# Optimization experiments

Hardware: AMD Instinct MI355X
Metric: run time of the kernel (lower is better)

## Reference

```python
import jax, jax.numpy as jnp
import numpy as np

B, LD, HD, CC, SC, PN, MAX_N = 256, 256, 512, 64, 256, 100000, 128


def setup_inputs() -> dict:
    key = jax.random.key(0)
    ks = jax.random.split(key, 24)
    def W(k, i, o):
        return jax.random.normal(k, (i, o), jnp.float32) * 0.02
    latent = jax.random.normal(ks[0], (B, LD), jnp.float32)
    n = jax.random.randint(ks[1], (B,), 0, MAX_N, jnp.int32)
    points = jax.random.normal(ks[2], (PN, SC), jnp.float32)
    a = jax.random.normal(ks[3], (PN, CC), jnp.float32)
    angles_params = a / (jnp.linalg.norm(a, axis=1, keepdims=True) + 1e-5)
    return {
        "latent": latent, "n": n, "points": points, "angles_params": angles_params,
        # angle_mlp: LD->HD->HD->HD->CC (4 linears, relu between)
        "aw1": W(ks[4], LD, HD), "ab1": jnp.zeros((HD,), jnp.float32),
        "aw2": W(ks[5], HD, HD), "ab2": jnp.zeros((HD,), jnp.float32),
        "aw3": W(ks[6], HD, HD), "ab3": jnp.zeros((HD,), jnp.float32),
        "aw4": W(ks[7], HD, CC), "ab4": jnp.zeros((CC,), jnp.float32),
        # lin1/lin2: 1 -> SC
        "l1w": W(ks[8], 1, SC), "l1b": jnp.zeros((SC,), jnp.float32),
        "l2w": W(ks[9], 1, SC), "l2b": jnp.zeros((SC,), jnp.float32),
        # out_lin: (SC+LD)->(SC+LD)->SC->SC
        "ow1": W(ks[10], SC + LD, SC + LD), "ob1": jnp.zeros((SC + LD,), jnp.float32),
        "ow2": W(ks[11], SC + LD, SC), "ob2": jnp.zeros((SC,), jnp.float32),
        "ow3": W(ks[12], SC, SC), "ob3": jnp.zeros((SC,), jnp.float32),
    }


def reference(latent, n, points, angles_params,
              aw1, ab1, aw2, ab2, aw3, ab3, aw4, ab4,
              l1w, l1b, l2w, l2b,
              ow1, ob1, ow2, ob2, ow3, ob3):
    n_r = jnp.clip(n, 1, MAX_N)  # round_n
    # angle_mlp
    h = jax.nn.relu(latent @ aw1 + ab1)
    h = jax.nn.relu(h @ aw2 + ab2)
    h = jax.nn.relu(h @ aw3 + ab3)
    ang = h @ aw4 + ab4                                   # [B, CC]
    ang = ang / (jnp.linalg.norm(ang, axis=1, keepdims=True) + 1e-5)
    cosine = jax.nn.softmax(ang @ angles_params.T, axis=1)  # [B, PN]
    srted, idx = jax.lax.top_k(cosine, MAX_N)             # sorted descending
    sel = points[idx]                                     # [B, MAX_N, SC] gather
    s = (MAX_N * srted)[..., None]                        # [B, MAX_N, 1]
    alpha = s @ l1w + l1b
    beta = s @ l2w + l2b
    mod = alpha * sel + beta                              # [B, MAX_N, SC]
    mask = (jnp.arange(MAX_N)[None, :] < n_r[:, None]).astype(jnp.float32)[..., None]
    cat = jnp.concatenate(
        [mod, jnp.broadcast_to(latent[:, None, :], (latent.shape[0], MAX_N, latent.shape[1]))],
        axis=-1)
    o = jax.nn.relu(cat @ ow1 + ob1)
    o = jax.nn.relu(o @ ow2 + ob2)
    out = o @ ow3 + ob3                                   # [B, MAX_N, SC]
    return out, mask, n_r
```

## Files before the change

### kernel.cpp

```cpp
#include <hip/hip_runtime.h>

#define PN 100000
#define NCB2 1563
#define NCBG 782
#define TSEL 0.33f
#define NSLOT 8
#define PREP_AP 3128
#define PREP_TOT 4408
#define PREP_CHUNK 1102

typedef _Float16 f16;
typedef _Float16 f16x8 __attribute__((ext_vector_type(8)));
typedef _Float16 f16x4 __attribute__((ext_vector_type(4)));
typedef float f32x4 __attribute__((ext_vector_type(4)));

__device__ __forceinline__ unsigned int sortkey(float f) {
    unsigned int u = __float_as_uint(f);
    return u ^ ((u & 0x80000000u) ? 0xFFFFFFFFu : 0x80000000u);
}

__device__ __forceinline__ void gload_lds16(const void* g, void* l) {
    __builtin_amdgcn_global_load_lds((const __attribute__((address_space(1))) void*)g,
                                     (__attribute__((address_space(3))) void*)l, 16, 0, 0);
}

__device__ __forceinline__ void prep_work(
    int pid, const float* __restrict__ ap, f16* __restrict__ apHpre, f16* __restrict__ apLpre,
    const float* __restrict__ ow1, const float* __restrict__ ow2, const float* __restrict__ ow3,
    f16* __restrict__ W1t, f16* __restrict__ W2t, f16* __restrict__ W3t)
{
    if (pid < PREP_AP) {
        int idx = pid * 256 + threadIdx.x;
        int gcol = idx >> 3, m = idx & 7;
        int bx = gcol >> 7, col = gcol & 127;
        size_t woff = (size_t)bx * 16384 + (size_t)col * 128 + (size_t)((m ^ (col & 7)) << 4);
        f16x8 h, l;
        if (gcol < PN) {
            const float* src = &ap[(size_t)gcol * 64 + m * 8];
            float4 a = *(const float4*)&src[0];
            float4 b = *(const float4*)&src[4];
            h[0] = (f16)a.x; l[0] = (f16)(a.x - (float)h[0]);
            h[1] = (f16)a.y; l[1] = (f16)(a.y - (float)h[1]);
            h[2] = (f16)a.z; l[2] = (f16)(a.z - (float)h[2]);
            h[3] = (f16)a.w; l[3] = (f16)(a.w - (float)h[3]);
            h[4] = (f16)b.x; l[4] = (f16)(b.x - (float)h[4]);
            h[5] = (f16)b.y; l[5] = (f16)(b.y - (float)h[5]);
            h[6] = (f16)b.z; l[6] = (f16)(b.z - (float)h[6]);
            h[7] = (f16)b.w; l[7] = (f16)(b.w - (float)h[7]);
        } else {
            h = (f16x8){}; l = (f16x8){};
        }
        *(f16x8*)((char*)apHpre + woff) = h;
        *(f16x8*)((char*)apLpre + woff) = l;
    } else {
        int idx = (pid - PREP_AP) * 256 + threadIdx.x;
        if (idx < 131072) {
            int n = idx >> 8, k = idx & 255;
            W1t[idx] = (f16)ow1[(size_t)k * 512 + n];
        } else if (idx < 262144) {
            int j = idx - 131072;
            int n = j >> 9, k = j & 511;
            W2t[j] = (f16)ow2[(size_t)k * 256 + n];
        } else {
            int j = idx - 262144;
            int n = j >> 8, k = j & 255;
            W3t[j] = (f16)ow3[(size_t)k * 256 + n];
        }
    }
}

template<int RELU>
__global__ __launch_bounds__(256) void k1_layer(
    const float* __restrict__ X, const float* __restrict__ W,
    const float* __restrict__ bias, float* __restrict__ Y,
    int N, int K, int prep_base,
    const float* __restrict__ ap, f16* __restrict__ apHpre, f16* __restrict__ apLpre,
    const float* __restrict__ ow1, const float* __restrict__ ow2, const float* __restrict__ ow3,
    f16* __restrict__ W1t, f16* __restrict__ W2t, f16* __restrict__ W3t)
{
    int bid = blockIdx.x;
    if (bid >= 64) {
        prep_work(prep_base + bid - 64, ap, apHpre, apLpre, ow1, ow2, ow3, W1t, W2t, W3t);
        return;
    }
    __shared__ __align__(16) float As[128][36];
    __shared__ __align__(16) float Bs[128][68];
    int t = threadIdx.x;
    int cbase = (bid & 7) * 64;
    int rbase = (bid >> 3) * 32;
    int tx = t & 15, ty = t >> 4;
    float acc[2][4] = {};

    for (int kt = 0; kt < K; kt += 128) {
        #pragma unroll
        for (int i = 0; i < 4; ++i) {
            int e = i * 256 + t;
            int r = e >> 5, k4 = e & 31;
            float4 v = *(const float4*)&X[(size_t)(rbase + r) * K + kt + k4 * 4];
            As[k4 * 4 + 0][r] = v.x; As[k4 * 4 + 1][r] = v.y;
            As[k4 * 4 + 2][r] = v.z; As[k4 * 4 + 3][r] = v.w;
        }
        #pragma unroll
        for (int i = 0; i < 8; ++i) {
            int e = i * 256 + t;
            int k = e >> 4, c4 = e & 15;
            *(float4*)&Bs[k][c4 * 4] = *(const float4*)&W[(size_t)(kt + k) * N + cbase + c4 * 4];
        }
        __syncthreads();
        #pragma unroll 8
        for (int k = 0; k < 128; ++k) {
            float2 av = *(const float2*)&As[k][ty * 2];
            float4 bv = *(const float4*)&Bs[k][tx * 4];
            acc[0][0] = fmaf(av.x, bv.x, acc[0][0]); acc[0][1] = fmaf(av.x, bv.y, acc[0][1]);
            acc[0][2] = fmaf(av.x, bv.z, acc[0][2]); acc[0][3] = fmaf(av.x, bv.w, acc[0][3]);
            acc[1][0] = fmaf(av.y, bv.x, acc[1][0]); acc[1][1] = fmaf(av.y, bv.y, acc[1][1]);
            acc[1][2] = fmaf(av.y, bv.z, acc[1][2]); acc[1][3] = fmaf(av.y, bv.w, acc[1][3]);
        }
        __syncthreads();
    }
    #pragma unroll
    for (int i = 0; i < 2; ++i) {
        int row = rbase + ty * 2 + i;
        #pragma unroll
        for (int j = 0; j < 4; ++j) {
            int col = cbase + tx * 4 + j;
            float v = acc[i][j] + bias[col];
            Y[(size_t)row * N + col] = RELU ? fmaxf(v, 0.f) : v;
        }
    }
}

__global__ __launch_bounds__(256) void k1_tail(
    const float* __restrict__ X, const float* __restrict__ W4,
    const float* __restrict__ b4, f16* __restrict__ angH, f16* __restrict__ angL,
    const float* __restrict__ latent, const float* __restrict__ ow1lat,
    const float* __restrict__ ob1, float* __restrict__ Lc, int prep_base,
    const float* __restrict__ ap, f16* __restrict__ apHpre, f16* __restrict__ apLpre,
    const float* __restrict__ ow1, const float* __restrict__ ow2, const float* __restrict__ ow3,
    f16* __restrict__ W1t, f16* __restrict__ W2t, f16* __restrict__ W3t)
{
    if (blockIdx.x >= 72) {
        prep_work(prep_base + blockIdx.x - 72, ap, apHpre, apLpre, ow1, ow2, ow3, W1t, W2t, W3t);
        return;
    }
    __shared__ __align__(16) float As[128][36];
    __shared__ __align__(16) float Bs[128][68];
    int t = threadIdx.x;
    int tx = t & 15, ty = t >> 4;
    float acc[2][4] = {};

    if (blockIdx.x < 8) {
        int rbase = blockIdx.x * 32;
        for (int kt = 0; kt < 512; kt += 128) {
            #pragma unroll
            for (int i = 0; i < 4; ++i) {
                int e = i * 256 + t;
                int r = e >> 5, k4 = e & 31;
                float4 v = *(const float4*)&X[(size_t)(rbase + r) * 512 + kt + k4 * 4];
                As[k4 * 4 + 0][r] = v.x; As[k4 * 4 + 1][r] = v.y;
                As[k4 * 4 + 2][r] = v.z; As[k4 * 4 + 3][r] = v.w;
            }
            #pragma unroll
            for (int i = 0; i < 8; ++i) {
                int e = i * 256 + t;
                int k = e >> 4, c4 = e & 15;
                *(float4*)&Bs[k][c4 * 4] = *(const float4*)&W4[(size_t)(kt + k) * 64 + c4 * 4];
            }
            __syncthreads();
            #pragma unroll 8
            for (int k = 0; k < 128; ++k) {
                float2 av = *(const float2*)&As[k][ty * 2];
                float4 bv = *(const float4*)&Bs[k][tx * 4];
                acc[0][0] = fmaf(av.x, bv.x, acc[0][0]); acc[0][1] = fmaf(av.x, bv.y, acc[0][1]);
                acc[0][2] = fmaf(av.x, bv.z, acc[0][2]); acc[0][3] = fmaf(av.x, bv.w, acc[0][3]);
                acc[1][0] = fmaf(av.y, bv.x, acc[1][0]); acc[1][1] = fmaf(av.y, bv.y, acc[1][1]);
                acc[1][2] = fmaf(av.y, bv.z, acc[1][2]); acc[1][3] = fmaf(av.y, bv.w, acc[1][3]);
            }
            __syncthreads();
        }
        #pragma unroll
        for (int i = 0; i < 2; ++i) {
            float v[4];
            float ss = 0.f;
            #pragma unroll
            for (int j = 0; j < 4; ++j) {
                v[j] = acc[i][j] + b4[tx * 4 + j];
                ss = fmaf(v[j], v[j], ss);
            }
            ss += __shfl_xor(ss, 1); ss += __shfl_xor(ss, 2);
            ss += __shfl_xor(ss, 4); ss += __shfl_xor(ss, 8);
            float inv = 1.0f / (sqrtf(ss) + 1e-5f);
            int row = rbase + ty * 2 + i;
            f16x4 h, l;
            #pragma unroll
            for (int j = 0; j < 4; ++j) {
                float val = v[j] * inv;
                h[j] = (f16)val;
                l[j] = (f16)(val - (float)h[j]);
            }
            *(f16x4*)&angH[(size_t)row * 64 + tx * 4] = h;
            *(f16x4*)&angL[(size_t)row * 64 + tx * 4] = l;
        }
    } else {
        int bid = blockIdx.x - 8;
        int cbase = (bid & 7) * 64;
        int rbase = (bid >> 3) * 32;
        for (int kt = 0; kt < 256; kt += 128) {
            #pragma unroll
            for (int i = 0; i < 4; ++i) {
                int e = i * 256 + t;
                int r = e >> 5, k4 = e & 31;
                float4 v = *(const float4*)&latent[(size_t)(rbase + r) * 256 + kt + k4 * 4];
                As[k4 * 4 + 0][r] = v.x; As[k4 * 4 + 1][r] = v.y;
                As[k4 * 4 + 2][r] = v.z; As[k4 * 4 + 3][r] = v.w;
            }
            #pragma unroll
            for (int i = 0; i < 8; ++i) {
                int e = i * 256 + t;
                int k = e >> 4, c4 = e & 15;
                *(float4*)&Bs[k][c4 * 4] = *(const float4*)&ow1lat[(size_t)(kt + k) * 512 + cbase + c4 * 4];
            }
            __syncthreads();
            #pragma unroll 8
            for (int k = 0; k < 128; ++k) {
                float2 av = *(const float2*)&As[k][ty * 2];
                float4 bv = *(const float4*)&Bs[k][tx * 4];
                acc[0][0] = fmaf(av.x, bv.x, acc[0][0]); acc[0][1] = fmaf(av.x, bv.y, acc[0][1]);
                acc[0][2] = fmaf(av.x, bv.z, acc[0][2]); acc[0][3] = fmaf(av.x, bv.w, acc[0][3]);
                acc[1][0] = fmaf(av.y, bv.x, acc[1][0]); acc[1][1] = fmaf(av.y, bv.y, acc[1][1]);
                acc[1][2] = fmaf(av.y, bv.z, acc[1][2]); acc[1][3] = fmaf(av.y, bv.w, acc[1][3]);
            }
            __syncthreads();
        }
        #pragma unroll
        for (int i = 0; i < 2; ++i) {
            int row = rbase + ty * 2 + i;
            #pragma unroll
            for (int j = 0; j < 4; ++j) {
                int col = cbase + tx * 4 + j;
                Lc[(size_t)row * 512 + col] = acc[i][j] + ob1[col];
            }
        }
    }
}

__global__ __launch_bounds__(256) void k2v10(
    const f16* __restrict__ angH, const f16* __restrict__ angL,
    const f16* __restrict__ apHpre, const f16* __restrict__ apLpre,
    float* __restrict__ gsum, unsigned int* __restrict__ cnt_g,
    unsigned long long* __restrict__ slot_g)
{
    __shared__ __align__(16) f16 Bh[128 * 64], Bl[128 * 64];
    __shared__ float psum[64][2];
    int t = threadIdx.x;
    int lane = t & 63, wave = t >> 6;
    int bx = blockIdx.x;
    int cbase = bx * 128;
    int rbase = blockIdx.y * 64;
    int wr = wave >> 1, wc = wave & 1;

    {
        const char* srcH = (const char*)apHpre + (size_t)bx * 16384 + t * 16;
        const char* srcL = (const char*)apLpre + (size_t)bx * 16384 + t * 16;
        char* dstH = (char*)Bh + wave * 1024;
        char* dstL = (char*)Bl + wave * 1024;
        #pragma unroll
        for (int c = 0; c < 4; ++c) {
            gload_lds16(srcH + c * 4096, dstH + c * 4096);
            gload_lds16(srcL + c * 4096, dstL + c * 4096);
        }
    }
    __syncthreads();

    f32x4 acc[2][4] = {};
    #pragma unroll
    for (int ks = 0; ks < 2; ++ks) {
        int kk = ks * 32 + (lane >> 4) * 8;
        f16x8 ah[2], al[2], bh[4], bl[4];
        #pragma unroll
        for (int i = 0; i < 2; ++i) {
            int row = rbase + wr * 32 + i * 16 + (lane & 15);
            ah[i] = *(const f16x8*)&angH[(size_t)row * 64 + kk];
            al[i] = *(const f16x8*)&angL[(size_t)row * 64 + kk];
        }
        #pragma unroll
        for (int j = 0; j < 4; ++j) {
            int col = wc * 64 + j * 16 + (lane & 15);
            unsigned int offb = (unsigned int)(col * 128 + kk * 2) ^ (unsigned int)((col & 7) << 4);
            bh[j] = *(const f16x8*)((char*)Bh + offb);
            bl[j] = *(const f16x8*)((char*)Bl + offb);
        }
        #pragma unroll
        for (int i = 0; i < 2; ++i)
            #pragma unroll
            for (int j = 0; j < 4; ++j) {
                acc[i][j] = __builtin_amdgcn_mfma_f32_16x16x32_f16(ah[i], bh[j], acc[i][j], 0, 0, 0);
                acc[i][j] = __builtin_amdgcn_mfma_f32_16x16x32_f16(ah[i], bl[j], acc[i][j], 0, 0, 0);
                acc[i][j] = __builtin_amdgcn_mfma_f32_16x16x32_f16(al[i], bh[j], acc[i][j], 0, 0, 0);
            }
    }

    int tx = lane & 15;
    #pragma unroll
    for (int i = 0; i < 2; ++i) {
        #pragma unroll
        for (int r2 = 0; r2 < 4; ++r2) {
            int lrow = wr * 32 + i * 16 + ((lane >> 4) << 2) + r2;
            int grow = rbase + lrow;
            float s = 0.f;
            unsigned int lk[4], li[4];
            int c = 0;
            #pragma unroll
            for (int j = 0; j < 4; ++j) {
                int gc = cbase + wc * 64 + j * 16 + tx;
                if (gc < PN) {
                    float v = acc[i][j][r2];
                    s += __expf(v);
                    if (v >= TSEL) { lk[c] = sortkey(v); li[c] = (unsigned int)gc; ++c; }
                }
            }
            s += __shfl_xor(s, 1); s += __shfl_xor(s, 2);
            s += __shfl_xor(s, 4); s += __shfl_xor(s, 8);
            int incl = c;
            #pragma unroll
            for (int d = 1; d < 16; d <<= 1) {
                int up = __shfl_up(incl, (unsigned int)d, 16);
                if (tx >= d) incl += up;
            }
            int excl = incl - c;
            int unit = bx * 2 + wc;
            if (unit < NCB2) {
                size_t base = ((size_t)unit * 256 + grow) * NSLOT;
                for (int k = 0; k < c; ++k) {
                    int sp = excl + k;
                    if (sp < NSLOT)
                        slot_g[base + sp] = (((unsigned long long)lk[k]) << 32) | (unsigned int)(~li[k]);
                }
                if (tx == 15) cnt_g[(size_t)unit * 256 + grow] = (unsigned int)incl;
            }
            if (tx == 0) psum[lrow][wc] = s;
        }
    }
    __syncthreads();
    if (t < 64)
        gsum[(size_t)bx * 256 + rbase + t] = psum[t][0] + psum[t][1];
}

__global__ __launch_bounds__(1024) void k3v5(
    const unsigned int* __restrict__ cnt_g, const unsigned long long* __restrict__ slot_g,
    const float* __restrict__ gsum, const int* __restrict__ nin,
    const float* __restrict__ points,
    const float* __restrict__ l1w, const float* __restrict__ l1b,
    const float* __restrict__ l2w, const float* __restrict__ l2b,
    f16* __restrict__ Xmod, float* __restrict__ maskp, float* __restrict__ nrp)
{
    __shared__ float wsum[16];
    __shared__ float s_inv;
    __shared__ unsigned int ccnt;
    __shared__ unsigned long long arr[1024];
    __shared__ float sprob[128];
    __shared__ int spi[128];
    __shared__ float sw1[256], sb1[256], sw2[256], sb2[256];

    int r = blockIdx.x;
    int t = threadIdx.x;
    if (t == 0) ccnt = 0u;
    if (t < 256) { sw1[t] = l1w[t]; sb1[t] = l1b[t]; sw2[t] = l2w[t]; sb2[t] = l2b[t]; }
    float es = 0.f;
    for (int i = t; i < NCBG; i += 1024) es += gsum[(size_t)i * 256 + r];
    #pragma unroll
    for (int off = 32; off > 0; off >>= 1) es += __shfl_xor(es, off);
    if ((t & 63) == 0) wsum[t >> 6] = es;
    __syncthreads();
    if (t == 0) {
        float s = 0.f;
        for (int i = 0; i < 16; ++i) s += wsum[i];
        s_inv = 1.0f / s;
    }
    for (int i = t; i < NCB2; i += 1024) {
        unsigned int c = cnt_g[(size_t)i * 256 + r];
        if (c) {
            c = min(c, (unsigned int)NSLOT);
            unsigned int p = atomicAdd(&ccnt, c);
            size_t base = ((size_t)i * 256 + r) * NSLOT;
            for (unsigned int k = 0; k < c; ++k)
                if (p + k < 1024u) arr[p + k] = slot_g[base + k];
        }
    }
    __syncthreads();
    int nc = (int)min(ccnt, 1024u);
    int P = 128;
    while (P < nc) P <<= 1;
    for (int i = t; i < P; i += 1024)
        if (i >= nc) arr[i] = 0ull;
    __syncthreads();
    for (int kk = 2; kk <= P; kk <<= 1) {
        for (int j = kk >> 1; j > 0; j >>= 1) {
            if (t < P) {
                int l = t ^ j;
                if (l > t) {
                    unsigned long long a = arr[t], b = arr[l];
                    bool up = ((t & kk) == 0);
                    if (up ? (a < b) : (a > b)) { arr[t] = b; arr[l] = a; }
                }
            }
            __syncthreads();
        }
    }
    int nr = nin[r]; nr = nr < 1 ? 1 : (nr > 128 ? 128 : nr);
    if (t < 128) {
        unsigned long long c = arr[t];
        unsigned int key = (unsigned int)(c >> 32);
        unsigned int idx = ~((unsigned int)c);
        if (idx >= PN) idx = 0;
        unsigned int u = (key & 0x80000000u) ? (key ^ 0x80000000u) : ~key;
        float v = __uint_as_float(u);
        sprob[t] = expf(v) * s_inv;
        spi[t] = (int)idx;
        maskp[r * 128 + t] = (t < nr) ? 1.0f : 0.0f;
    }
    if (t == 0) nrp[r] = (float)nr;
    __syncthreads();
    {
        int tok = t >> 3;
        int d0 = (t & 7) * 32;
        float s = 128.0f * sprob[tok];
        const float* prow = points + (size_t)spi[tok] * 256;
        f16* xrow = Xmod + ((size_t)(r * 128 + tok)) * 256;
        #pragma unroll
        for (int j = 0; j < 32; j += 4) {
            int d = d0 + j;
            float4 p = *(const float4*)&prow[d];
            f16x4 h;
            h[0] = (f16)fmaf(fmaf(s, sw1[d + 0], sb1[d + 0]), p.x, fmaf(s, sw2[d + 0], sb2[d + 0]));
            h[1] = (f16)fmaf(fmaf(s, sw1[d + 1], sb1[d + 1]), p.y, fmaf(s, sw2[d + 1], sb2[d + 1]));
            h[2] = (f16)fmaf(fmaf(s, sw1[d + 2], sb1[d + 2]), p.z, fmaf(s, sw2[d + 2], sb2[d + 2]));
            h[3] = (f16)fmaf(fmaf(s, sw1[d + 3], sb1[d + 3]), p.w, fmaf(s, sw2[d + 3], sb2[d + 3]));
            *(f16x4*)&xrow[d] = h;
        }
    }
}

template<int RELU, int OUT_F16, int LCBIAS>
__global__ __launch_bounds__(256) void gemm_tn3(
    const f16* __restrict__ A, const f16* __restrict__ Bt,
    const float* __restrict__ bias,
    f16* __restrict__ Cf16, float* __restrict__ Cf32,
    int N, int K)
{
    __shared__ __align__(16) f16 As[64 * 64];
    __shared__ __align__(16) f16 Bs[128 * 64];
    int tid = threadIdx.x;
    int lane = tid & 63, wave = tid >> 6;
    int brow = blockIdx.y * 64;
    int bcol = blockIdx.x * 128;
    int wr = wave >> 1, wc = wave & 1;

    f32x4 acc[2][4] = {};

    int sr = tid >> 3;
    int soff = (tid & 7) * 16;
    char* ldsA = (char*)As + wave * 1024;
    char* ldsB = (char*)Bs + wave * 1024;

    for (int kt = 0; kt < K; kt += 64) {
        #pragma unroll
        for (int c = 0; c < 2; ++c) {
            int r = sr + c * 32;
            const char* ga = (const char*)A + ((size_t)(brow + r) * K + kt) * 2 + soff;
            gload_lds16(ga, ldsA + c * 4096);
        }
        #pragma unroll
        for (int c = 0; c < 4; ++c) {
            int r = sr + c * 32;
            const char* gb = (const char*)Bt + ((size_t)(bcol + r) * K + kt) * 2 + soff;
            gload_lds16(gb, ldsB + c * 4096);
        }
        __syncthreads();
        #pragma unroll
        for (int ks = 0; ks < 2; ++ks) {
            f16x8 af[2], bf[4];
            int kk = ks * 32 + (lane >> 4) * 8;
            #pragma unroll
            for (int i = 0; i < 2; ++i) {
                int row = wr * 32 + i * 16 + (lane & 15);
                af[i] = *(const f16x8*)&As[row * 64 + kk];
            }
            #pragma unroll
            for (int j = 0; j < 4; ++j) {
                int col = wc * 64 + j * 16 + (lane & 15);
                bf[j] = *(const f16x8*)&Bs[col * 64 + kk];
            }
            #pragma unroll
            for (int i = 0; i < 2; ++i)
                #pragma unroll
                for (int j = 0; j < 4; ++j)
                    acc[i][j] = __builtin_amdgcn_mfma_f32_16x16x32_f16(af[i], bf[j], acc[i][j], 0, 0, 0);
        }
        __syncthreads();
    }

    #pragma unroll
    for (int i = 0; i < 2; ++i) {
        int row0 = brow + wr * 32 + i * 16 + (lane >> 4) * 4;
        #pragma unroll
        for (int j = 0; j < 4; ++j) {
            int col = bcol + wc * 64 + j * 16 + (lane & 15);
            float bz = LCBIAS ? bias[(size_t)(row0 >> 7) * N + col] : bias[col];
            #pragma unroll
            for (int r2 = 0; r2 < 4; ++r2) {
                float v = acc[i][j][r2] + bz;
                if (RELU) v = fmaxf(v, 0.f);
                if (OUT_F16) Cf16[(size_t)(row0 + r2) * N + col] = (f16)v;
                else         Cf32[(size_t)(row0 + r2) * N + col] = v;
            }
        }
    }
}

extern "C" void kernel_launch(void* const* d_in, const int* in_sizes, int n_in,
                              void* d_out, int out_size, void* d_ws, size_t ws_size,
                              hipStream_t stream) {
    (void)in_sizes; (void)n_in; (void)out_size; (void)ws_size;
    const float* latent = (const float*)d_in[0];
    const int*   nin    = (const int*)d_in[1];
    const float* points = (const float*)d_in[2];
    const float* ap     = (const float*)d_in[3];
    const float* aw1 = (const float*)d_in[4];  const float* ab1 = (const float*)d_in[5];
    const float* aw2 = (const float*)d_in[6];  const float* ab2 = (const float*)d_in[7];
    const float* aw3 = (const float*)d_in[8];  const float* ab3 = (const float*)d_in[9];
    const float* aw4 = (const float*)d_in[10]; const float* ab4 = (const float*)d_in[11];
    const float* l1w = (const float*)d_in[12]; const float* l1b = (const float*)d_in[13];
    const float* l2w = (const float*)d_in[14]; const float* l2b = (const float*)d_in[15];
    const float* ow1 = (const float*)d_in[16]; const float* ob1 = (const float*)d_in[17];
    const float* ow2 = (const float*)d_in[18]; const float* ob2 = (const float*)d_in[19];
    const float* ow3 = (const float*)d_in[20]; const float* ob3 = (const float*)d_in[21];

    char* wsb = (char*)d_ws;
    f16* angH  = (f16*)wsb;
    f16* angL  = (f16*)(wsb + 65536);
    unsigned int* cnt_g = (unsigned int*)(wsb + 1048576);
    float* gsum   = (float*)(wsb + 3145728);
    float* h1 = (float*)(wsb + 5242880);
    float* h2 = (float*)(wsb + 5767168);
    float* h3 = (float*)(wsb + 6291456);
    float* Lc = (float*)(wsb + 6815744);
    f16* apHpre = (f16*)(wsb + 8388608);
    f16* Xmod = (f16*)(wsb + 8388608);
    unsigned long long* slot_g = (unsigned long long*)(wsb + 25165824);
    f16* H1  = (f16*)(wsb + 25165824);
    f16* apLpre = (f16*)(wsb + 58720256);
    f16* H2  = (f16*)(wsb + 58720256);
    f16* W1t = (f16*)(wsb + 75497472);
    f16* W2t = (f16*)(wsb + 75759616);
    f16* W3t = (f16*)(wsb + 76021760);

    float* outp  = (float*)d_out;
    float* maskp = outp + 8388608;
    float* nrp   = outp + 8421376;

    hipLaunchKernelGGL((k1_layer<1>), dim3(64 + PREP_CHUNK), dim3(256), 0, stream,
                       latent, aw1, ab1, h1, 512, 256, 0,
                       ap, apHpre, apLpre, ow1, ow2, ow3, W1t, W2t, W3t);
    hipLaunchKernelGGL((k1_layer<1>), dim3(64 + PREP_CHUNK), dim3(256), 0, stream,
                       h1, aw2, ab2, h2, 512, 512, PREP_CHUNK,
                       ap, apHpre, apLpre, ow1, ow2, ow3, W1t, W2t, W3t);
    hipLaunchKernelGGL((k1_layer<1>), dim3(64 + PREP_CHUNK), dim3(256), 0, stream,
                       h2, aw3, ab3, h3, 512, 512, 2 * PREP_CHUNK,
                       ap, apHpre, apLpre, ow1, ow2, ow3, W1t, W2t, W3t);
    hipLaunchKernelGGL(k1_tail, dim3(72 + PREP_CHUNK), dim3(256), 0, stream,
                       h3, aw4, ab4, angH, angL,
                       latent, ow1 + (size_t)256 * 512, ob1, Lc, 3 * PREP_CHUNK,
                       ap, apHpre, apLpre, ow1, ow2, ow3, W1t, W2t, W3t);
    hipLaunchKernelGGL(k2v10, dim3(NCBG, 4), dim3(256), 0, stream,
                       angH, angL, apHpre, apLpre, gsum, cnt_g, slot_g);
    hipLaunchKernelGGL(k3v5, dim3(256), dim3(1024), 0, stream,
                       cnt_g, slot_g, gsum, nin, points, l1w, l1b, l2w, l2b,
                       Xmod, maskp, nrp);
    hipLaunchKernelGGL((gemm_tn3<1, 1, 1>), dim3(4, 512), dim3(256), 0, stream,
                       Xmod, W1t, Lc, H1, (float*)nullptr, 512, 256);
    hipLaunchKernelGGL((gemm_tn3<1, 1, 0>), dim3(2, 512), dim3(256), 0, stream,
                       H1, W2t, ob2, H2, (float*)nullptr, 256, 512);
    hipLaunchKernelGGL((gemm_tn3<0, 0, 0>), dim3(2, 512), dim3(256), 0, stream,
                       H2, W3t, ob3, (f16*)nullptr, outp, 256, 256);
}
```

Before: 183.6 us.

## Fuse four angle-MLP layer kernels into one per-row-block kernel

Replaces the three k1_layer launches and k1_tail with a single k_mlp kernel. Each of 64 blocks owns 4 latent rows and computes all four MLP layers plus the latent part of out_lin layer 1, keeping activations in LDS. The prep work is now done by extra blocks in this same launch. This removes three launches and the global round trips for h1-h3, at the cost of each block re-reading every weight matrix from global/L2 with no LDS tiling and a long serial dependency chain per block.

```diff
diff --git a/kernel.cpp b/kernel.cpp
--- a/kernel.cpp
+++ b/kernel.cpp
@@ -7,7 +7,6 @@
 #define NSLOT 8
 #define PREP_AP 3128
 #define PREP_TOT 4408
-#define PREP_CHUNK 1102
 
 typedef _Float16 f16;
 typedef _Float16 f16x8 __attribute__((ext_vector_type(8)));
@@ -69,178 +68,145 @@
     }
 }
 
-template<int RELU>
-__global__ __launch_bounds__(256) void k1_layer(
-    const float* __restrict__ X, const float* __restrict__ W,
-    const float* __restrict__ bias, float* __restrict__ Y,
-    int N, int K, int prep_base,
+__global__ __launch_bounds__(256) void k_mlp(
+    const float* __restrict__ latent,
+    const float* __restrict__ aw1, const float* __restrict__ ab1,
+    const float* __restrict__ aw2, const float* __restrict__ ab2,
+    const float* __restrict__ aw3, const float* __restrict__ ab3,
+    const float* __restrict__ aw4, const float* __restrict__ ab4,
+    const float* __restrict__ ow1lat, const float* __restrict__ ob1,
+    f16* __restrict__ angH, f16* __restrict__ angL, float* __restrict__ Lc,
     const float* __restrict__ ap, f16* __restrict__ apHpre, f16* __restrict__ apLpre,
     const float* __restrict__ ow1, const float* __restrict__ ow2, const float* __restrict__ ow3,
     f16* __restrict__ W1t, f16* __restrict__ W2t, f16* __restrict__ W3t)
 {
     int bid = blockIdx.x;
     if (bid >= 64) {
-        prep_work(prep_base + bid - 64, ap, apHpre, apLpre, ow1, ow2, ow3, W1t, W2t, W3t);
+        prep_work(bid - 64, ap, apHpre, apLpre, ow1, ow2, ow3, W1t, W2t, W3t);
         return;
     }
-    __shared__ __align__(16) float As[128][36];
-    __shared__ __align__(16) float Bs[128][68];
+    __shared__ __align__(16) float xs[4][512];
+    __shared__ __align__(16) float ns[4][512];
     int t = threadIdx.x;
-    int cbase = (bid & 7) * 64;
-    int rbase = (bid >> 3) * 32;
-    int tx = t & 15, ty = t >> 4;
-    float acc[2][4] = {};
-
-    for (int kt = 0; kt < K; kt += 128) {
-        #pragma unroll
-        for (int i = 0; i < 4; ++i) {
-            int e = i * 256 + t;
-            int r = e >> 5, k4 = e & 31;
-            float4 v = *(const float4*)&X[(size_t)(rbase + r) * K + kt + k4 * 4];
-            As[k4 * 4 + 0][r] = v.x; As[k4 * 4 + 1][r] = v.y;
-            As[k4 * 4 + 2][r] = v.z; As[k4 * 4 + 3][r] = v.w;
-        }
-        #pragma unroll
-        for (int i = 0; i < 8; ++i) {
-            int e = i * 256 + t;
-            int k = e >> 4, c4 = e & 15;
-            *(float4*)&Bs[k][c4 * 4] = *(const float4*)&W[(size_t)(kt + k) * N + cbase + c4 * 4];
-        }
-        __syncthreads();
-        #pragma unroll 8
-        for (int k = 0; k < 128; ++k) {
-            float2 av = *(const float2*)&As[k][ty * 2];
-            float4 bv = *(const float4*)&Bs[k][tx * 4];
-            acc[0][0] = fmaf(av.x, bv.x, acc[0][0]); acc[0][1] = fmaf(av.x, bv.y, acc[0][1]);
-            acc[0][2] = fmaf(av.x, bv.z, acc[0][2]); acc[0][3] = fmaf(av.x, bv.w, acc[0][3]);
-            acc[1][0] = fmaf(av.y, bv.x, acc[1][0]); acc[1][1] = fmaf(av.y, bv.y, acc[1][1]);
-            acc[1][2] = fmaf(av.y, bv.z, acc[1][2]); acc[1][3] = fmaf(av.y, bv.w, acc[1][3]);
-        }
-        __syncthreads();
-    }
-    #pragma unroll
-    for (int i = 0; i < 2; ++i) {
-        int row = rbase + ty * 2 + i;
-        #pragma unroll
-        for (int j = 0; j < 4; ++j) {
-            int col = cbase + tx * 4 + j;
-            float v = acc[i][j] + bias[col];
-            Y[(size_t)row * N + col] = RELU ? fmaxf(v, 0.f) : v;
-        }
-    }
-}
-
-__global__ __launch_bounds__(256) void k1_tail(
-    const float* __restrict__ X, const float* __restrict__ W4,
-    const float* __restrict__ b4, f16* __restrict__ angH, f16* __restrict__ angL,
-    const float* __restrict__ latent, const float* __restrict__ ow1lat,
-    const float* __restrict__ ob1, float* __restrict__ Lc, int prep_base,
-    const float* __restrict__ ap, f16* __restrict__ apHpre, f16* __restrict__ apLpre,
-    const float* __restrict__ ow1, const float* __restrict__ ow2, const float* __restrict__ ow3,
-    f16* __restrict__ W1t, f16* __restrict__ W2t, f16* __restrict__ W3t)
-{
-    if (blockIdx.x >= 72) {
-        prep_work(prep_base + blockIdx.x - 72, ap, apHpre, apLpre, ow1, ow2, ow3, W1t, W2t, W3t);
-        return;
-    }
-    __shared__ __align__(16) float As[128][36];
-    __shared__ __align__(16) float Bs[128][68];
-    int t = threadIdx.x;
-    int tx = t & 15, ty = t >> 4;
-    float acc[2][4] = {};
-
-    if (blockIdx.x < 8) {
-        int rbase = blockIdx.x * 32;
-        for (int kt = 0; kt < 512; kt += 128) {
-            #pragma unroll
-            for (int i = 0; i < 4; ++i) {
-                int e = i * 256 + t;
-                int r = e >> 5, k4 = e & 31;
-                float4 v = *(const float4*)&X[(size_t)(rbase + r) * 512 + kt + k4 * 4];
-                As[k4 * 4 + 0][r] = v.x; As[k4 * 4 + 1][r] = v.y;
-                As[k4 * 4 + 2][r] = v.z; As[k4 * 4 + 3][r] = v.w;
-            }
-            #pragma unroll
-            for (int i = 0; i < 8; ++i) {
-                int e = i * 256 + t;
-                int k = e >> 4, c4 = e & 15;
-                *(float4*)&Bs[k][c4 * 4] = *(const float4*)&W4[(size_t)(kt + k) * 64 + c4 * 4];
-            }
-            __syncthreads();
-            #pragma unroll 8
-            for (int k = 0; k < 128; ++k) {
-                float2 av = *(const float2*)&As[k][ty * 2];
-                float4 bv = *(const float4*)&Bs[k][tx * 4];
-                acc[0][0] = fmaf(av.x, bv.x, acc[0][0]); acc[0][1] = fmaf(av.x, bv.y, acc[0][1]);
-                acc[0][2] = fmaf(av.x, bv.z, acc[0][2]); acc[0][3] = fmaf(av.x, bv.w, acc[0][3]);
-                acc[1][0] = fmaf(av.y, bv.x, acc[1][0]); acc[1][1] = fmaf(av.y, bv.y, acc[1][1]);
-                acc[1][2] = fmaf(av.y, bv.z, acc[1][2]); acc[1][3] = fmaf(av.y, bv.w, acc[1][3]);
-            }
-            __syncthreads();
-        }
-        #pragma unroll
-        for (int i = 0; i < 2; ++i) {
-            float v[4];
-            float ss = 0.f;
-            #pragma unroll
-            for (int j = 0; j < 4; ++j) {
-                v[j] = acc[i][j] + b4[tx * 4 + j];
-                ss = fmaf(v[j], v[j], ss);
-            }
-            ss += __shfl_xor(ss, 1); ss += __shfl_xor(ss, 2);
-            ss += __shfl_xor(ss, 4); ss += __shfl_xor(ss, 8);
-            float inv = 1.0f / (sqrtf(ss) + 1e-5f);
-            int row = rbase + ty * 2 + i;
-            f16x4 h, l;
-            #pragma unroll
-            for (int j = 0; j < 4; ++j) {
-                float val = v[j] * inv;
-                h[j] = (f16)val;
-                l[j] = (f16)(val - (float)h[j]);
-            }
-            *(f16x4*)&angH[(size_t)row * 64 + tx * 4] = h;
-            *(f16x4*)&angL[(size_t)row * 64 + tx * 4] = l;
-        }
-    } else {
-        int bid = blockIdx.x - 8;
-        int cbase = (bid & 7) * 64;
-        int rbase = (bid >> 3) * 32;
-        for (int kt = 0; kt < 256; kt += 128) {
-            #pragma unroll
-            for (int i = 0; i < 4; ++i) {
-                int e = i * 256 + t;
-                int r = e >> 5, k4 = e & 31;
-                float4 v = *(const float4*)&latent[(size_t)(rbase + r) * 256 + kt + k4 * 4];
-                As[k4 * 4 + 0][r] = v.x; As[k4 * 4 + 1][r] = v.y;
-                As[k4 * 4 + 2][r] = v.z; As[k4 * 4 + 3][r] = v.w;
-            }
-            #pragma unroll
-            for (int i = 0; i < 8; ++i) {
-                int e = i * 256 + t;
-                int k = e >> 4, c4 = e & 15;
-                *(float4*)&Bs[k][c4 * 4] = *(const float4*)&ow1lat[(size_t)(kt + k) * 512 + cbase + c4 * 4];
-            }
-            __syncthreads();
-            #pragma unroll 8
-            for (int k = 0; k < 128; ++k) {
-                float2 av = *(const float2*)&As[k][ty * 2];
-                float4 bv = *(const float4*)&Bs[k][tx * 4];
-                acc[0][0] = fmaf(av.x, bv.x, acc[0][0]); acc[0][1] = fmaf(av.x, bv.y, acc[0][1]);
-                acc[0][2] = fmaf(av.x, bv.z, acc[0][2]); acc[0][3] = fmaf(av.x, bv.w, acc[0][3]);
-                acc[1][0] = fmaf(av.y, bv.x, acc[1][0]); acc[1][1] = fmaf(av.y, bv.y, acc[1][1]);
-                acc[1][2] = fmaf(av.y, bv.z, acc[1][2]); acc[1][3] = fmaf(av.y, bv.w, acc[1][3]);
-            }
-            __syncthreads();
-        }
-        #pragma unroll
-        for (int i = 0; i < 2; ++i) {
-            int row = rbase + ty * 2 + i;
-            #pragma unroll
-            for (int j = 0; j < 4; ++j) {
-                int col = cbase + tx * 4 + j;
-                Lc[(size_t)row * 512 + col] = acc[i][j] + ob1[col];
-            }
-        }
+    int r0 = bid * 4;
+    {
+        int row = t >> 6, c4 = (t & 63) * 4;
+        *(float4*)&xs[row][c4] = *(const float4*)&latent[(size_t)(r0 + row) * 256 + c4];
+    }
+    __syncthreads();
+
+    #pragma unroll
+    for (int p = 0; p < 2; ++p) {
+        int col = p * 256 + t;
+        float a0 = 0.f, a1 = 0.f, a2 = 0.f, a3 = 0.f;
+        float c0 = 0.f, c1 = 0.f, c2 = 0.f, c3 = 0.f;
+        for (int k = 0; k < 256; k += 4) {
+            float4 x0 = *(const float4*)&xs[0][k];
+            float4 x1 = *(const float4*)&xs[1][k];
+            float4 x2 = *(const float4*)&xs[2][k];
+            float4 x3 = *(const float4*)&xs[3][k];
+            float w0 = aw1[(size_t)(k + 0) * 512 + col];
+            float w1 = aw1[(size_t)(k + 1) * 512 + col];
+            float w2 = aw1[(size_t)(k + 2) * 512 + col];
+            float w3 = aw1[(size_t)(k + 3) * 512 + col];
+            a0 = fmaf(x0.x, w0, a0); a0 = fmaf(x0.y, w1, a0); a0 = fmaf(x0.z, w2, a0); a0 = fmaf(x0.w, w3, a0);
+            a1 = fmaf(x1.x, w0, a1); a1 = fmaf(x1.y, w1, a1); a1 = fmaf(x1.z, w2, a1); a1 = fmaf(x1.w, w3, a1);
+            a2 = fmaf(x2.x, w0, a2); a2 = fmaf(x2.y, w1, a2); a2 = fmaf(x2.z, w2, a2); a2 = fmaf(x2.w, w3, a2);
+            a3 = fmaf(x3.x, w0, a3); a3 = fmaf(x3.y, w1, a3); a3 = fmaf(x3.z, w2, a3); a3 = fmaf(x3.w, w3, a3);
+            float v0 = ow1lat[(size_t)(k + 0) * 512 + col];
+            float v1 = ow1lat[(size_t)(k + 1) * 512 + col];
+            float v2 = ow1lat[(size_t)(k + 2) * 512 + col];
+            float v3 = ow1lat[(size_t)(k + 3) * 512 + col];
+            c0 = fmaf(x0.x, v0, c0); c0 = fmaf(x0.y, v1, c0); c0 = fmaf(x0.z, v2, c0); c0 = fmaf(x0.w, v3, c0);
+            c1 = fmaf(x1.x, v0, c1); c1 = fmaf(x1.y, v1, c1); c1 = fmaf(x1.z, v2, c1); c1 = fmaf(x1.w, v3, c1);
+            c2 = fmaf(x2.x, v0, c2); c2 = fmaf(x2.y, v1, c2); c2 = fmaf(x2.z, v2, c2); c2 = fmaf(x2.w, v3, c2);
+            c3 = fmaf(x3.x, v0, c3); c3 = fmaf(x3.y, v1, c3); c3 = fmaf(x3.z, v2, c3); c3 = fmaf(x3.w, v3, c3);
+        }
+        float b1 = ab1[col];
+        ns[0][col] = fmaxf(a0 + b1, 0.f);
+        ns[1][col] = fmaxf(a1 + b1, 0.f);
+        ns[2][col] = fmaxf(a2 + b1, 0.f);
+        ns[3][col] = fmaxf(a3 + b1, 0.f);
+        float bo = ob1[col];
+        Lc[(size_t)(r0 + 0) * 512 + col] = c0 + bo;
+        Lc[(size_t)(r0 + 1) * 512 + col] = c1 + bo;
+        Lc[(size_t)(r0 + 2) * 512 + col] = c2 + bo;
+        Lc[(size_t)(r0 + 3) * 512 + col] = c3 + bo;
+    }
+    __syncthreads();
+
+    #pragma unroll
+    for (int p = 0; p < 2; ++p) {
+        int col = p * 256 + t;
+        float a0 = 0.f, a1 = 0.f, a2 = 0.f, a3 = 0.f;
+        for (int k = 0; k < 512; k += 4) {
+            float4 x0 = *(const float4*)&ns[0][k];
+            float4 x1 = *(const float4*)&ns[1][k];
+            float4 x2 = *(const float4*)&ns[2][k];
+            float4 x3 = *(const float4*)&ns[3][k];
+            float w0 = aw2[(size_t)(k + 0) * 512 + col];
+            float w1 = aw2[(size_t)(k + 1) * 512 + col];
+            float w2 = aw2[(size_t)(k + 2) * 512 + col];
+            float w3 = aw2[(size_t)(k + 3) * 512 + col];
+            a0 = fmaf(x0.x, w0, a0); a0 = fmaf(x0.y, w1, a0); a0 = fmaf(x0.z, w2, a0); a0 = fmaf(x0.w, w3, a0);
+            a1 = fmaf(x1.x, w0, a1); a1 = fmaf(x1.y, w1, a1); a1 = fmaf(x1.z, w2, a1); a1 = fmaf(x1.w, w3, a1);
+            a2 = fmaf(x2.x, w0, a2); a2 = fmaf(x2.y, w1, a2); a2 = fmaf(x2.z, w2, a2); a2 = fmaf(x2.w, w3, a2);
+            a3 = fmaf(x3.x, w0, a3); a3 = fmaf(x3.y, w1, a3); a3 = fmaf(x3.z, w2, a3); a3 = fmaf(x3.w, w3, a3);
+        }
+        float bz = ab2[col];
+        xs[0][col] = fmaxf(a0 + bz, 0.f);
+        xs[1][col] = fmaxf(a1 + bz, 0.f);
+        xs[2][col] = fmaxf(a2 + bz, 0.f);
+        xs[3][col] = fmaxf(a3 + bz, 0.f);
+    }
+    __syncthreads();
+
+    #pragma unroll
+    for (int p = 0; p < 2; ++p) {
+        int col = p * 256 + t;
+        float a0 = 0.f, a1 = 0.f, a2 = 0.f, a3 = 0.f;
+        for (int k = 0; k < 512; k += 4) {
+            float4 x0 = *(const float4*)&xs[0][k];
+            float4 x1 = *(const float4*)&xs[1][k];
+            float4 x2 = *(const float4*)&xs[2][k];
+            float4 x3 = *(const float4*)&xs[3][k];
+            float w0 = aw3[(size_t)(k + 0) * 512 + col];
+            float w1 = aw3[(size_t)(k + 1) * 512 + col];
+            float w2 = aw3[(size_t)(k + 2) * 512 + col];
+            float w3 = aw3[(size_t)(k + 3) * 512 + col];
+            a0 = fmaf(x0.x, w0, a0); a0 = fmaf(x0.y, w1, a0); a0 = fmaf(x0.z, w2, a0); a0 = fmaf(x0.w, w3, a0);
+            a1 = fmaf(x1.x, w0, a1); a1 = fmaf(x1.y, w1, a1); a1 = fmaf(x1.z, w2, a1); a1 = fmaf(x1.w, w3, a1);
+            a2 = fmaf(x2.x, w0, a2); a2 = fmaf(x2.y, w1, a2); a2 = fmaf(x2.z, w2, a2); a2 = fmaf(x2.w, w3, a2);
+            a3 = fmaf(x3.x, w0, a3); a3 = fmaf(x3.y, w1, a3); a3 = fmaf(x3.z, w2, a3); a3 = fmaf(x3.w, w3, a3);
+        }
+        float bz = ab3[col];
+        ns[0][col] = fmaxf(a0 + bz, 0.f);
+        ns[1][col] = fmaxf(a1 + bz, 0.f);
+        ns[2][col] = fmaxf(a2 + bz, 0.f);
+        ns[3][col] = fmaxf(a3 + bz, 0.f);
+    }
+    __syncthreads();
+
+    {
+        int row = t >> 6, col = t & 63;
+        float acc = 0.f;
+        for (int k = 0; k < 512; k += 4) {
+            float4 x = *(const float4*)&ns[row][k];
+            acc = fmaf(x.x, aw4[(size_t)(k + 0) * 64 + col], acc);
+            acc = fmaf(x.y, aw4[(size_t)(k + 1) * 64 + col], acc);
+            acc = fmaf(x.z, aw4[(size_t)(k + 2) * 64 + col], acc);
+            acc = fmaf(x.w, aw4[(size_t)(k + 3) * 64 + col], acc);
+        }
+        float v = acc + ab4[col];
+        float ss = v * v;
+        #pragma unroll
+        for (int off = 32; off > 0; off >>= 1) ss += __shfl_xor(ss, off);
+        float inv = 1.0f / (sqrtf(ss) + 1e-5f);
+        float val = v * inv;
+        f16 h = (f16)val;
+        f16 l = (f16)(val - (float)h);
+        angH[(size_t)(r0 + row) * 64 + col] = h;
+        angL[(size_t)(r0 + row) * 64 + col] = l;
     }
 }
 
@@ -541,9 +507,6 @@
     f16* angL  = (f16*)(wsb + 65536);
     unsigned int* cnt_g = (unsigned int*)(wsb + 1048576);
     float* gsum   = (float*)(wsb + 3145728);
-    float* h1 = (float*)(wsb + 5242880);
-    float* h2 = (float*)(wsb + 5767168);
-    float* h3 = (float*)(wsb + 6291456);
     float* Lc = (float*)(wsb + 6815744);
     f16* apHpre = (f16*)(wsb + 8388608);
     f16* Xmod = (f16*)(wsb + 8388608);
@@ -559,18 +522,9 @@
     float* maskp = outp + 8388608;
     float* nrp   = outp + 8421376;
 
-    hipLaunchKernelGGL((k1_layer<1>), dim3(64 + PREP_CHUNK), dim3(256), 0, stream,
-                       latent, aw1, ab1, h1, 512, 256, 0,
-                       ap, apHpre, apLpre, ow1, ow2, ow3, W1t, W2t, W3t);
-    hipLaunchKernelGGL((k1_layer<1>), dim3(64 + PREP_CHUNK), dim3(256), 0, stream,
-                       h1, aw2, ab2, h2, 512, 512, PREP_CHUNK,
-                       ap, apHpre, apLpre, ow1, ow2, ow3, W1t, W2t, W3t);
-    hipLaunchKernelGGL((k1_layer<1>), dim3(64 + PREP_CHUNK), dim3(256), 0, stream,
-                       h2, aw3, ab3, h3, 512, 512, 2 * PREP_CHUNK,
-                       ap, apHpre, apLpre, ow1, ow2, ow3, W1t, W2t, W3t);
-    hipLaunchKernelGGL(k1_tail, dim3(72 + PREP_CHUNK), dim3(256), 0, stream,
-                       h3, aw4, ab4, angH, angL,
-                       latent, ow1 + (size_t)256 * 512, ob1, Lc, 3 * PREP_CHUNK,
+    hipLaunchKernelGGL(k_mlp, dim3(64 + PREP_TOT), dim3(256), 0, stream,
+                       latent, aw1, ab1, aw2, ab2, aw3, ab3, aw4, ab4,
+                       ow1 + (size_t)256 * 512, ob1, angH, angL, Lc,
                        ap, apHpre, apLpre, ow1, ow2, ow3, W1t, W2t, W3t);
     hipLaunchKernelGGL(k2v10, dim3(NCBG, 4), dim3(256), 0, stream,
                        angH, angL, apHpre, apLpre, gsum, cnt_g, slot_g);
```

New measurement: 246.9 us. +34.5%, slower.
